# Performance work log

Hardware: AMD Instinct MI355X
Metric: run time of the kernel (lower is better)

The kernel has to match this reference:

```python
import jax, jax.numpy as jnp
import numpy as np

E = 1024   # embed_size
H = 16     # heads
D = E // H # head_dim = 64
F = 4 * E  # ffn hidden = 4096
N, S = 4, 2048
EPS = 1e-5


def _layernorm(x, w, b):
    m = jnp.mean(x, axis=-1, keepdims=True)
    v = jnp.var(x, axis=-1, keepdims=True)
    return (x - m) * jax.lax.rsqrt(v + EPS) * w + b


def setup_inputs() -> dict:
    key = jax.random.key(0)
    ks = jax.random.split(key, 10)
    s = 0.02
    return {
        "x": jax.random.normal(ks[0], (N, S, E), dtype=jnp.float32),
        "Wq": jax.random.normal(ks[1], (E, E), dtype=jnp.float32) * s,
        "Wk": jax.random.normal(ks[2], (E, E), dtype=jnp.float32) * s,
        "Wv": jax.random.normal(ks[3], (E, E), dtype=jnp.float32) * s,
        "Wo": jax.random.normal(ks[4], (E, E), dtype=jnp.float32) * s,
        "bo": jnp.zeros((E,), dtype=jnp.float32),
        "ln1_w": jnp.ones((E,), dtype=jnp.float32),
        "ln1_b": jnp.zeros((E,), dtype=jnp.float32),
        "ln2_w": jnp.ones((E,), dtype=jnp.float32),
        "ln2_b": jnp.zeros((E,), dtype=jnp.float32),
        "W1": jax.random.normal(ks[5], (F, E), dtype=jnp.float32) * s,
        "bf1": jnp.zeros((F,), dtype=jnp.float32),
        "W2": jax.random.normal(ks[6], (E, F), dtype=jnp.float32) * s,
        "bf2": jnp.zeros((E,), dtype=jnp.float32),
    }


def reference(x, Wq, Wk, Wv, Wo, bo, ln1_w, ln1_b, ln2_w, ln2_b, W1, bf1, W2, bf2):
    n, s, _ = x.shape
    # projections (torch Linear: x @ W.T), no bias for q/k/v
    q = (x @ Wq.T).reshape(n, s, H, D).transpose(0, 2, 1, 3)  # (N,H,S,D)
    k = (x @ Wk.T).reshape(n, s, H, D).transpose(0, 2, 1, 3)
    v = (x @ Wv.T).reshape(n, s, H, D).transpose(0, 2, 1, 3)
    # NOTE: faithful to original einsum strings applied to permuted tensors.
    # energy: (N, H, H, S)
    energy = jnp.einsum('nqhd,nkhd->nqkh', q, k)
    attention = jax.nn.softmax(energy / jnp.sqrt(jnp.float32(D)), axis=3)
    # out: (N, H, S, D); k and v axes each summed independently (as in torch)
    out = jnp.einsum('nqkh,nvhd->nqhd', attention, v).reshape(n, s, E)
    attn = out @ Wo.T + bo
    # residual + LN1 (dropout is identity in eval mode)
    x = _layernorm(attn + x, ln1_w, ln1_b)
    # FFN
    ff = jnp.maximum(x @ W1.T + bf1, 0.0) @ W2.T + bf2
    x = _layernorm(ff + x, ln2_w, ln2_b)
    return x
```

## Files before the change

### kernel.cpp

```cpp
#include <hip/hip_runtime.h>

typedef __attribute__((ext_vector_type(8))) __bf16 bf16x8;
typedef __attribute__((ext_vector_type(8))) unsigned short us8;
typedef __attribute__((ext_vector_type(4))) float f32x4;

#define DEV __device__ __forceinline__

DEV unsigned short f2bf(float f) {
    unsigned u = __builtin_bit_cast(unsigned, f);
    u += 0x7fffu + ((u >> 16) & 1u);
    return (unsigned short)(u >> 16);
}
DEV float bf2f(unsigned short h) {
    return __builtin_bit_cast(float, (unsigned)h << 16);
}

DEV void gload_lds16(const void* g, void* l) {
    __builtin_amdgcn_global_load_lds(
        (const __attribute__((address_space(1))) unsigned int*)g,
        (__attribute__((address_space(3))) unsigned int*)l, 16, 0, 0);
}

#define VMCNT8 asm volatile("s_waitcnt vmcnt(8)" ::: "memory")
#define VMCNT0 asm volatile("s_waitcnt vmcnt(0)" ::: "memory")
#define BAR __builtin_amdgcn_s_barrier()

template <int EPI>
__global__ __launch_bounds__(512) void gemm256(
    const unsigned short* __restrict__ A, const unsigned short* __restrict__ B,
    void* __restrict__ Cv, const float* __restrict__ bias,
    int lda, int ldb, int N, int Kslice) {
    extern __shared__ char smem[];
    const int t = threadIdx.x;
    const int m0 = blockIdx.y * 256;
    const int n0 = blockIdx.x * 256;
    const int z = blockIdx.z;
    const unsigned short* Ag = A + (size_t)z * Kslice;
    const unsigned short* Bg = B + (size_t)z * Kslice;
    const int NT = Kslice >> 6;

    size_t aoff[4], boff[4];
    int ldb_off[4];
#pragma unroll
    for (int j = 0; j < 4; ++j) {
        int cj = j * 512 + t;
        int row = cj >> 3, slot = cj & 7;
        int col = (slot ^ (row & 7)) << 3;
        aoff[j] = (size_t)(m0 + row) * lda + col;
        boff[j] = (size_t)(n0 + row) * ldb + col;
        ldb_off[j] = cj << 4;
    }

    const int lane = t & 63, r = lane & 15, g = lane >> 4;
    const int wid = t >> 6, wm = wid >> 2, wn = wid & 3;
    const int s0 = (g ^ (r & 7)) << 4;
    const int aRow = (wm * 128 + r) * 128;
    const int bRow = (wn * 64 + r) * 128;

#define LDA8(base, mi, kk) \
    (*(const bf16x8*)((base) + aRow + (mi) * 2048 + (s0 ^ ((kk) << 6))))
#define LDB8(base, ni, kk) \
    (*(const bf16x8*)((base) + 32768 + bRow + (ni) * 2048 + (s0 ^ ((kk) << 6))))

#define STAGE(base, kt)                                                       \
    do {                                                                      \
        const unsigned short* _as = Ag + (size_t)(kt) * 64;                   \
        const unsigned short* _bs = Bg + (size_t)(kt) * 64;                   \
        _Pragma("unroll") for (int j = 0; j < 4; ++j)                         \
            gload_lds16(_as + aoff[j], (base) + ldb_off[j]);                  \
        _Pragma("unroll") for (int j = 0; j < 4; ++j)                         \
            gload_lds16(_bs + boff[j], (base) + 32768 + ldb_off[j]);          \
    } while (0)

#define PHASE_BODY(MH)                                                        \
    BAR;                                                                      \
    asm volatile("s_waitcnt lgkmcnt(0)" ::: "memory");                        \
    __builtin_amdgcn_sched_barrier(0);                                        \
    __builtin_amdgcn_s_setprio(1);                                            \
    _Pragma("unroll") for (int q = 0; q < 4; ++q)                             \
        _Pragma("unroll") for (int ni = 0; ni < 4; ++ni)                      \
            acc[(MH) * 4 + q][ni] = __builtin_amdgcn_mfma_f32_16x16x32_bf16(  \
                af[q], bfr[ni], acc[(MH) * 4 + q][ni], 0, 0, 0);              \
    __builtin_amdgcn_s_setprio(0);

#define COMPUTE_TILE(base)                                                    \
    do {                                                                      \
        _Pragma("unroll") for (int kk = 0; kk < 2; ++kk) {                    \
            bf16x8 bfr[4], af[4];                                             \
            _Pragma("unroll") for (int ni = 0; ni < 4; ++ni)                  \
                bfr[ni] = LDB8(base, ni, kk);                                 \
            _Pragma("unroll") for (int q = 0; q < 4; ++q)                     \
                af[q] = LDA8(base, q, kk);                                    \
            PHASE_BODY(0)                                                     \
            BAR;                                                              \
            _Pragma("unroll") for (int q = 0; q < 4; ++q)                     \
                af[q] = LDA8(base, 4 + q, kk);                                \
            PHASE_BODY(1)                                                     \
        }                                                                     \
        BAR;                                                                  \
    } while (0)

    f32x4 acc[8][4] = {};
    char* buf0 = smem;
    char* buf1 = smem + 65536;

    STAGE(buf0, 0);
    STAGE(buf1, 1);
    VMCNT8;
    BAR;

    for (int kt = 0; kt < NT; kt += 2) {
        COMPUTE_TILE(buf0);
        if (kt + 2 < NT) {
            STAGE(buf0, kt + 2);
            VMCNT8;
        } else {
            VMCNT0;
        }
        BAR;
        COMPUTE_TILE(buf1);
        if (kt + 3 < NT) {
            STAGE(buf1, kt + 3);
            VMCNT8;
        } else {
            VMCNT0;
        }
        BAR;
    }

    const int crow0 = m0 + wm * 128 + g * 4;
    const int ccol0 = n0 + wn * 64 + r;
    float* Cp = (float*)Cv + (size_t)gridDim.y * 256 * N * z;
#pragma unroll
    for (int mi = 0; mi < 8; ++mi) {
#pragma unroll
        for (int ni = 0; ni < 4; ++ni) {
            int col = ccol0 + ni * 16;
            float bval = (EPI == 2) ? bias[col] : 0.f;
#pragma unroll
            for (int j = 0; j < 4; ++j) {
                int row = crow0 + mi * 16 + j;
                float v = acc[mi][ni][j];
                if (EPI == 0) {
                    ((unsigned short*)Cv)[(size_t)row * N + col] = f2bf(v);
                } else if (EPI == 1) {
                    Cp[(size_t)row * N + col] = v;
                } else {
                    v = fmaxf(v + bval, 0.f);
                    ((unsigned short*)Cv)[(size_t)row * N + col] = f2bf(v);
                }
            }
        }
    }
#undef LDA8
#undef LDB8
#undef STAGE
#undef PHASE_BODY
#undef COMPUTE_TILE
}

__global__ __launch_bounds__(256) void cvt_kernel(
    const float* __restrict__ in, unsigned short* __restrict__ out, int n4) {
    int idx = blockIdx.x * 256 + threadIdx.x;
    if (idx >= n4) return;
    float4 v = *(const float4*)(in + (size_t)idx * 4);
    ushort4 u = make_ushort4(f2bf(v.x), f2bf(v.y), f2bf(v.z), f2bf(v.w));
    *(ushort4*)(out + (size_t)idx * 4) = u;
}

__global__ __launch_bounds__(256) void energy_kernel(
    const unsigned short* __restrict__ QKV, float* __restrict__ E) {
    __shared__ __attribute__((aligned(16))) unsigned short Qs[8 * 1024];
    __shared__ __attribute__((aligned(16))) unsigned short Ks[8 * 1024];
    const int tid = threadIdx.x;
    const int n = blockIdx.y;
    const int s0 = blockIdx.x * 8;
#pragma unroll
    for (int c = 0; c < 4; ++c) {
        int e = c * 2048 + tid * 8;
        int row = e >> 10, col = e & 1023;
        int jj = col >> 6, db = (col >> 3) & 7;
        int sw = jj * 64 + (((db + jj) & 7) << 3);
        size_t gbase = (size_t)(n * 2048 + s0 + row) * 3072;
        *(us8*)(Qs + row * 1024 + sw) = *(const us8*)(QKV + gbase + col);
        *(us8*)(Ks + row * 1024 + sw) = *(const us8*)(QKV + gbase + 1024 + col);
    }
    __syncthreads();
    const int i = tid >> 4, j = tid & 15;
#pragma unroll
    for (int s = 0; s < 8; ++s) {
        float acc = 0.f;
#pragma unroll
        for (int d8 = 0; d8 < 8; ++d8) {
            us8 q = *(const us8*)(Qs + s * 1024 + i * 64 + (((d8 + i) & 7) << 3));
            us8 k = *(const us8*)(Ks + s * 1024 + j * 64 + (((d8 + j) & 7) << 3));
#pragma unroll
            for (int t = 0; t < 8; ++t) acc += bf2f(q[t]) * bf2f(k[t]);
        }
        E[(size_t)(n * 2048 + s0 + s) * 256 + tid] = acc * 0.125f;
    }
}

__global__ __launch_bounds__(256) void smax_part(
    const float* __restrict__ E, float* __restrict__ Mp, float* __restrict__ Zp) {
    const int p = threadIdx.x, n = blockIdx.y, sc = blockIdx.x;
    float m = -1e30f, z = 0.f;
    const float* base = E + ((size_t)n * 2048 + sc * 128) * 256 + p;
    for (int s = 0; s < 128; ++s) {
        float e = base[(size_t)s * 256];
        float mn = fmaxf(m, e);
        z = z * __expf(m - mn) + __expf(e - mn);
        m = mn;
    }
    int idx = (n * 16 + sc) * 256 + p;
    Mp[idx] = m;
    Zp[idx] = z;
}

__global__ __launch_bounds__(256) void smax_fin(
    const float* __restrict__ Mp, const float* __restrict__ Zp,
    float* __restrict__ Mf, float* __restrict__ RZf) {
    const int p = threadIdx.x, n = blockIdx.x;
    float m = -1e30f;
    for (int c = 0; c < 16; ++c) m = fmaxf(m, Mp[(n * 16 + c) * 256 + p]);
    float z = 0.f;
    for (int c = 0; c < 16; ++c)
        z += Zp[(n * 16 + c) * 256 + p] * __expf(Mp[(n * 16 + c) * 256 + p] - m);
    Mf[n * 256 + p] = m;
    RZf[n * 256 + p] = 1.f / z;
}

__global__ __launch_bounds__(256) void attnsrc_kernel(
    const unsigned short* __restrict__ QKV, const float* __restrict__ E,
    const float* __restrict__ Mf, const float* __restrict__ RZf,
    unsigned short* __restrict__ ASRC) {
    const int lane = threadIdx.x & 63;
    const int widx = blockIdx.x * 4 + (threadIdx.x >> 6);
    const int n = widx >> 11, s = widx & 2047;
    float vs = 0.f;
    const unsigned short* vrow = QKV + (size_t)(n * 2048 + s) * 3072 + 2048;
#pragma unroll
    for (int h = 0; h < 16; ++h) vs += bf2f(vrow[h * 64 + lane]);
    float aval = 0.f;
    if (lane < 16) {
        const float* erow = E + (size_t)(n * 2048 + s) * 256 + lane * 16;
        const float* mrow = Mf + n * 256 + lane * 16;
        const float* zrow = RZf + n * 256 + lane * 16;
#pragma unroll
        for (int j = 0; j < 16; ++j)
            aval += __expf(erow[j] - mrow[j]) * zrow[j];
    }
#pragma unroll
    for (int h = 0; h < 16; ++h) {
        float ah = __shfl(aval, h, 64);
        size_t row = (size_t)n * 2048 + h * 128 + (s >> 4);
        ASRC[row * 1024 + (s & 15) * 64 + lane] = f2bf(ah * vs);
    }
}

__global__ __launch_bounds__(256) void ln_kernel(
    const float* __restrict__ lin, const float* __restrict__ lin2,
    const float* __restrict__ bias, const float* __restrict__ resid,
    const float* __restrict__ w, const float* __restrict__ b,
    unsigned short* __restrict__ obf, float* __restrict__ of) {
    __shared__ float sm[16];
    const int row = blockIdx.x, c = threadIdx.x * 4;
    const size_t off = (size_t)row * 1024 + c;
    float4 v = *(const float4*)(lin + off);
    float4 bs = *(const float4*)(bias + c);
    float4 rx = *(const float4*)(resid + off);
    float t0 = v.x + bs.x + rx.x;
    float t1 = v.y + bs.y + rx.y;
    float t2 = v.z + bs.z + rx.z;
    float t3 = v.w + bs.w + rx.w;
    if (lin2) {
        float4 v2 = *(const float4*)(lin2 + off);
        t0 += v2.x; t1 += v2.y; t2 += v2.z; t3 += v2.w;
    }
    float s = t0 + t1 + t2 + t3;
    float ss = t0 * t0 + t1 * t1 + t2 * t2 + t3 * t3;
#pragma unroll
    for (int o = 32; o > 0; o >>= 1) {
        s += __shfl_down(s, o, 64);
        ss += __shfl_down(ss, o, 64);
    }
    const int wv = threadIdx.x >> 6, ln = threadIdx.x & 63;
    if (ln == 0) {
        sm[wv] = s;
        sm[8 + wv] = ss;
    }
    __syncthreads();
    if (threadIdx.x == 0) {
        sm[4] = sm[0] + sm[1] + sm[2] + sm[3];
        sm[12] = sm[8] + sm[9] + sm[10] + sm[11];
    }
    __syncthreads();
    s = sm[4];
    ss = sm[12];
    float mean = s * (1.f / 1024.f);
    float var = ss * (1.f / 1024.f) - mean * mean;
    float rstd = rsqrtf(var + 1e-5f);
    float4 wv4 = *(const float4*)(w + c);
    float4 bv4 = *(const float4*)(b + c);
    float o0 = (t0 - mean) * rstd * wv4.x + bv4.x;
    float o1 = (t1 - mean) * rstd * wv4.y + bv4.y;
    float o2 = (t2 - mean) * rstd * wv4.z + bv4.z;
    float o3 = (t3 - mean) * rstd * wv4.w + bv4.w;
    if (of) {
        float4 o = make_float4(o0, o1, o2, o3);
        *(float4*)(of + off) = o;
    }
    if (obf) {
        ushort4 u = make_ushort4(f2bf(o0), f2bf(o1), f2bf(o2), f2bf(o3));
        *(ushort4*)(obf + off) = u;
    }
}

extern "C" void kernel_launch(void* const* d_in, const int* in_sizes, int n_in,
                              void* d_out, int out_size, void* d_ws, size_t ws_size,
                              hipStream_t stream) {
    const float* x = (const float*)d_in[0];
    const float* Wq = (const float*)d_in[1];
    const float* Wk = (const float*)d_in[2];
    const float* Wv = (const float*)d_in[3];
    const float* Wo = (const float*)d_in[4];
    const float* bo = (const float*)d_in[5];
    const float* ln1w = (const float*)d_in[6];
    const float* ln1b = (const float*)d_in[7];
    const float* ln2w = (const float*)d_in[8];
    const float* ln2b = (const float*)d_in[9];
    const float* W1 = (const float*)d_in[10];
    const float* bf1 = (const float*)d_in[11];
    const float* W2 = (const float*)d_in[12];
    const float* bf2 = (const float*)d_in[13];

    char* ws = (char*)d_ws;
    const size_t MB = 1u << 20;
    unsigned short* W1bf = (unsigned short*)(ws + 0);
    unsigned short* W2bf = (unsigned short*)(ws + 8 * MB);
    unsigned short* Wobf = (unsigned short*)(ws + 16 * MB);
    unsigned short* Wqkvbf = (unsigned short*)(ws + 18 * MB);
    float* Mp = (float*)(ws + 24 * MB);
    float* Zp = (float*)(ws + 24 * MB + 64 * 1024);
    float* Mfin = (float*)(ws + 24 * MB + 128 * 1024);
    float* RZfin = (float*)(ws + 24 * MB + 160 * 1024);
    float* x1f = (float*)(ws + 16 * MB);
    unsigned short* ASRC = (unsigned short*)(ws + 48 * MB);
    unsigned short* x1bf = (unsigned short*)(ws + 48 * MB);
    float* AL = (float*)(ws + 64 * MB);
    unsigned short* H1 = (unsigned short*)(ws + 64 * MB);
    unsigned short* QKV = (unsigned short*)(ws + 128 * MB);
    float* FF = (float*)(ws + 128 * MB);
    unsigned short* xbf = (unsigned short*)(ws + 176 * MB);
    float* EN = (float*)(ws + 176 * MB);

    auto k0 = gemm256<0>; auto k1 = gemm256<1>; auto k2 = gemm256<2>;
    (void)hipFuncSetAttribute((const void*)k0, hipFuncAttributeMaxDynamicSharedMemorySize, 131072);
    (void)hipFuncSetAttribute((const void*)k1, hipFuncAttributeMaxDynamicSharedMemorySize, 131072);
    (void)hipFuncSetAttribute((const void*)k2, hipFuncAttributeMaxDynamicSharedMemorySize, 131072);

    auto cvt = [&](const float* src, unsigned short* dst, int n) {
        int n4 = n >> 2;
        cvt_kernel<<<dim3((n4 + 255) / 256), dim3(256), 0, stream>>>(src, dst, n4);
    };
    cvt(x, xbf, 8192 * 1024);
    cvt(Wq, Wqkvbf, 1024 * 1024);
    cvt(Wk, Wqkvbf + 1024 * 1024, 1024 * 1024);
    cvt(Wv, Wqkvbf + 2 * 1024 * 1024, 1024 * 1024);
    cvt(Wo, Wobf, 1024 * 1024);
    cvt(W1, W1bf, 4096 * 1024);
    cvt(W2, W2bf, 4096 * 1024);

    gemm256<0><<<dim3(12, 32, 1), 512, 131072, stream>>>(
        xbf, Wqkvbf, QKV, nullptr, 1024, 1024, 3072, 1024);
    energy_kernel<<<dim3(256, 4), 256, 0, stream>>>(QKV, EN);
    smax_part<<<dim3(16, 4), 256, 0, stream>>>(EN, Mp, Zp);
    smax_fin<<<dim3(4), 256, 0, stream>>>(Mp, Zp, Mfin, RZfin);
    attnsrc_kernel<<<dim3(2048), 256, 0, stream>>>(QKV, EN, Mfin, RZfin, ASRC);
    gemm256<1><<<dim3(4, 32, 2), 512, 131072, stream>>>(
        ASRC, Wobf, AL, nullptr, 1024, 1024, 1024, 512);
    ln_kernel<<<dim3(8192), 256, 0, stream>>>(
        AL, AL + (size_t)8192 * 1024, bo, x, ln1w, ln1b, x1bf, x1f);
    gemm256<2><<<dim3(16, 32, 1), 512, 131072, stream>>>(
        x1bf, W1bf, H1, bf1, 1024, 1024, 4096, 1024);
    gemm256<1><<<dim3(4, 32, 2), 512, 131072, stream>>>(
        H1, W2bf, FF, nullptr, 4096, 4096, 1024, 2048);
    ln_kernel<<<dim3(8192), 256, 0, stream>>>(
        FF, FF + (size_t)8192 * 1024, bf2, x1f, ln2w, ln2b, nullptr, (float*)d_out);
}
```

Baseline: 460.8 us.

## Restructure GEMM mainloop to 4-stage K=32 pipeline with interleaved loads and block swizzle

The 256x256 bf16 GEMM mainloop moves from a 2-buffer, 64-wide K tile to a 4-slot ring of 32-wide K tiles with three tiles in flight. The A and B global-to-LDS loads for tile kt+3 are split across the two MFMA phases so memory traffic overlaps compute. The LDS swizzle is changed to match the narrower rows. Workgroup IDs are also remapped with a modulo-8 permutation, likely to spread neighbouring tiles across XCDs for better L2 locality. In exchange there are more barriers per unit of K work and a shallower MFMA batch per tile.

```diff
diff --git a/kernel.cpp b/kernel.cpp
--- a/kernel.cpp
+++ b/kernel.cpp
@@ -22,8 +22,12 @@
 }
 
 #define VMCNT8 asm volatile("s_waitcnt vmcnt(8)" ::: "memory")
+#define VMCNT4 asm volatile("s_waitcnt vmcnt(4)" ::: "memory")
 #define VMCNT0 asm volatile("s_waitcnt vmcnt(0)" ::: "memory")
 #define BAR __builtin_amdgcn_s_barrier()
+#define LGKM0                                          \
+    asm volatile("s_waitcnt lgkmcnt(0)" ::: "memory"); \
+    __builtin_amdgcn_sched_barrier(0)
 
 template <int EPI>
 __global__ __launch_bounds__(512) void gemm256(
@@ -32,100 +36,103 @@
     int lda, int ldb, int N, int Kslice) {
     extern __shared__ char smem[];
     const int t = threadIdx.x;
-    const int m0 = blockIdx.y * 256;
-    const int n0 = blockIdx.x * 256;
-    const int z = blockIdx.z;
+
+    const int gx = gridDim.x, gy = gridDim.y;
+    const int total = gx * gy * gridDim.z;
+    int flat = blockIdx.x + gx * (blockIdx.y + gy * blockIdx.z);
+    flat = (flat & 7) * (total >> 3) + (flat >> 3);
+    const int bx = flat % gx;
+    const int byz = flat / gx;
+    const int by = byz % gy;
+    const int z = byz / gy;
+
+    const int m0 = by * 256, n0 = bx * 256;
     const unsigned short* Ag = A + (size_t)z * Kslice;
     const unsigned short* Bg = B + (size_t)z * Kslice;
-    const int NT = Kslice >> 6;
-
-    size_t aoff[4], boff[4];
-    int ldb_off[4];
-#pragma unroll
-    for (int j = 0; j < 4; ++j) {
+    const int NT = Kslice >> 5;
+
+    size_t aoff[2], boff[2];
+    int loff[2];
+#pragma unroll
+    for (int j = 0; j < 2; ++j) {
         int cj = j * 512 + t;
-        int row = cj >> 3, slot = cj & 7;
-        int col = (slot ^ (row & 7)) << 3;
+        int row = cj >> 2, slot = cj & 3;
+        int col = (slot ^ ((row >> 1) & 3)) << 3;
         aoff[j] = (size_t)(m0 + row) * lda + col;
         boff[j] = (size_t)(n0 + row) * ldb + col;
-        ldb_off[j] = cj << 4;
+        loff[j] = cj << 4;
     }
 
     const int lane = t & 63, r = lane & 15, g = lane >> 4;
     const int wid = t >> 6, wm = wid >> 2, wn = wid & 3;
-    const int s0 = (g ^ (r & 7)) << 4;
-    const int aRow = (wm * 128 + r) * 128;
-    const int bRow = (wn * 64 + r) * 128;
-
-#define LDA8(base, mi, kk) \
-    (*(const bf16x8*)((base) + aRow + (mi) * 2048 + (s0 ^ ((kk) << 6))))
-#define LDB8(base, ni, kk) \
-    (*(const bf16x8*)((base) + 32768 + bRow + (ni) * 2048 + (s0 ^ ((kk) << 6))))
-
-#define STAGE(base, kt)                                                       \
-    do {                                                                      \
-        const unsigned short* _as = Ag + (size_t)(kt) * 64;                   \
-        const unsigned short* _bs = Bg + (size_t)(kt) * 64;                   \
-        _Pragma("unroll") for (int j = 0; j < 4; ++j)                         \
-            gload_lds16(_as + aoff[j], (base) + ldb_off[j]);                  \
-        _Pragma("unroll") for (int j = 0; j < 4; ++j)                         \
-            gload_lds16(_bs + boff[j], (base) + 32768 + ldb_off[j]);          \
+    const int s0 = (g ^ ((r >> 1) & 3)) << 4;
+    const int aRowB = (wm * 128 + r) * 64 + s0;
+    const int bRowB = 16384 + (wn * 64 + r) * 64 + s0;
+
+#define LDA8(buf, mi) (*(const bf16x8*)((buf) + aRowB + (mi) * 1024))
+#define LDB8(buf, ni) (*(const bf16x8*)((buf) + bRowB + (ni) * 1024))
+#define STAGE_A(buf, kt)                                                  \
+    do {                                                                  \
+        _Pragma("unroll") for (int j = 0; j < 2; ++j)                     \
+            gload_lds16(Ag + aoff[j] + (size_t)(kt) * 32, (buf) + loff[j]); \
     } while (0)
-
-#define PHASE_BODY(MH)                                                        \
-    BAR;                                                                      \
-    asm volatile("s_waitcnt lgkmcnt(0)" ::: "memory");                        \
-    __builtin_amdgcn_sched_barrier(0);                                        \
-    __builtin_amdgcn_s_setprio(1);                                            \
-    _Pragma("unroll") for (int q = 0; q < 4; ++q)                             \
-        _Pragma("unroll") for (int ni = 0; ni < 4; ++ni)                      \
-            acc[(MH) * 4 + q][ni] = __builtin_amdgcn_mfma_f32_16x16x32_bf16(  \
-                af[q], bfr[ni], acc[(MH) * 4 + q][ni], 0, 0, 0);              \
-    __builtin_amdgcn_s_setprio(0);
-
-#define COMPUTE_TILE(base)                                                    \
-    do {                                                                      \
-        _Pragma("unroll") for (int kk = 0; kk < 2; ++kk) {                    \
-            bf16x8 bfr[4], af[4];                                             \
-            _Pragma("unroll") for (int ni = 0; ni < 4; ++ni)                  \
-                bfr[ni] = LDB8(base, ni, kk);                                 \
-            _Pragma("unroll") for (int q = 0; q < 4; ++q)                     \
-                af[q] = LDA8(base, q, kk);                                    \
-            PHASE_BODY(0)                                                     \
-            BAR;                                                              \
-            _Pragma("unroll") for (int q = 0; q < 4; ++q)                     \
-                af[q] = LDA8(base, 4 + q, kk);                                \
-            PHASE_BODY(1)                                                     \
-        }                                                                     \
-        BAR;                                                                  \
+#define STAGE_B(buf, kt)                                                  \
+    do {                                                                  \
+        _Pragma("unroll") for (int j = 0; j < 2; ++j)                     \
+            gload_lds16(Bg + boff[j] + (size_t)(kt) * 32,                 \
+                        (buf) + 16384 + loff[j]);                         \
     } while (0)
 
     f32x4 acc[8][4] = {};
-    char* buf0 = smem;
-    char* buf1 = smem + 65536;
-
-    STAGE(buf0, 0);
-    STAGE(buf1, 1);
-    VMCNT8;
-    BAR;
-
-    for (int kt = 0; kt < NT; kt += 2) {
-        COMPUTE_TILE(buf0);
-        if (kt + 2 < NT) {
-            STAGE(buf0, kt + 2);
+
+    STAGE_A(smem, 0);
+    STAGE_B(smem, 0);
+    STAGE_A(smem + 32768, 1);
+    STAGE_B(smem + 32768, 1);
+    STAGE_A(smem + 65536, 2);
+    STAGE_B(smem + 65536, 2);
+
+    for (int kt = 0; kt < NT; ++kt) {
+        if (kt < NT - 2) {
             VMCNT8;
+        } else if (kt == NT - 2) {
+            VMCNT4;
         } else {
             VMCNT0;
         }
         BAR;
-        COMPUTE_TILE(buf1);
-        if (kt + 3 < NT) {
-            STAGE(buf1, kt + 3);
-            VMCNT8;
-        } else {
-            VMCNT0;
-        }
+        char* buf = smem + (kt & 3) * 32768;
+        char* nbuf = smem + ((kt + 3) & 3) * 32768;
+        const bool st = (kt + 3) < NT;
+        bf16x8 bfr[4], af[4];
+#pragma unroll
+        for (int ni = 0; ni < 4; ++ni) bfr[ni] = LDB8(buf, ni);
+#pragma unroll
+        for (int q = 0; q < 4; ++q) af[q] = LDA8(buf, q);
+        if (st) STAGE_A(nbuf, kt + 3);
         BAR;
+        LGKM0;
+        __builtin_amdgcn_s_setprio(1);
+#pragma unroll
+        for (int q = 0; q < 4; ++q)
+#pragma unroll
+            for (int ni = 0; ni < 4; ++ni)
+                acc[q][ni] = __builtin_amdgcn_mfma_f32_16x16x32_bf16(
+                    af[q], bfr[ni], acc[q][ni], 0, 0, 0);
+        __builtin_amdgcn_s_setprio(0);
+#pragma unroll
+        for (int q = 0; q < 4; ++q) af[q] = LDA8(buf, 4 + q);
+        if (st) STAGE_B(nbuf, kt + 3);
+        BAR;
+        LGKM0;
+        __builtin_amdgcn_s_setprio(1);
+#pragma unroll
+        for (int q = 0; q < 4; ++q)
+#pragma unroll
+            for (int ni = 0; ni < 4; ++ni)
+                acc[4 + q][ni] = __builtin_amdgcn_mfma_f32_16x16x32_bf16(
+                    af[q], bfr[ni], acc[4 + q][ni], 0, 0, 0);
+        __builtin_amdgcn_s_setprio(0);
     }
 
     const int crow0 = m0 + wm * 128 + g * 4;
@@ -154,9 +161,8 @@
     }
 #undef LDA8
 #undef LDB8
-#undef STAGE
-#undef PHASE_BODY
-#undef COMPUTE_TILE
+#undef STAGE_A
+#undef STAGE_B
 }
 
 __global__ __launch_bounds__(256) void cvt_kernel(
```

Result: no change. 468.0 us (+1.6%).
